# Optimization experiments

Measured on AMD Instinct MI355X. Metric: run time of the kernel, lower is better.

## Reference

```python
import jax, jax.numpy as jnp
import numpy as np

D_MODEL = 2048
HEADS = 16


def setup_inputs() -> dict:
    key = jax.random.key(0)
    ks = jax.random.split(key, 9)
    s = 1.0 / np.sqrt(D_MODEL)
    x = jax.random.normal(ks[0], (2, 2048, D_MODEL), dtype=jnp.float32)
    wq = jax.random.uniform(ks[1], (D_MODEL, D_MODEL), jnp.float32, -s, s)
    wk = jax.random.uniform(ks[2], (D_MODEL, D_MODEL), jnp.float32, -s, s)
    wv = jax.random.uniform(ks[3], (D_MODEL, D_MODEL), jnp.float32, -s, s)
    wo = jax.random.uniform(ks[4], (D_MODEL, D_MODEL), jnp.float32, -s, s)
    bq = jax.random.uniform(ks[5], (D_MODEL,), jnp.float32, -s, s)
    bk = jax.random.uniform(ks[6], (D_MODEL,), jnp.float32, -s, s)
    bv = jax.random.uniform(ks[7], (D_MODEL,), jnp.float32, -s, s)
    bo = jax.random.uniform(ks[8], (D_MODEL,), jnp.float32, -s, s)
    return {"x": x, "wq": wq, "bq": bq, "wk": wk, "bk": bk,
            "wv": wv, "bv": bv, "wo": wo, "bo": bo}


def _split(t, heads):
    b, s, d = t.shape
    return t.reshape(b, s, heads, d // heads).transpose(0, 2, 1, 3)  # [b,h,s,dh]


def reference(x, wq, bq, wk, bk, wv, bv, wo, bo):
    q = x @ wq.T + bq
    k = x @ wk.T + bk
    v = x @ wv.T + bv
    q, k, v = _split(q, HEADS), _split(k, HEADS), _split(v, HEADS)
    dh = q.shape[-1]
    scale = 1.0 / np.sqrt(dh).astype(np.float32)
    score = jnp.einsum('bhqd,bhkd->bhqk', q, k) * scale  # [b,h,s,s]
    score = jax.nn.softmax(score.astype(jnp.float32), axis=-1).astype(q.dtype)
    out = jnp.einsum('bhqk,bhkd->bhqd', score, v)
    b, h, s, _ = out.shape
    out = out.transpose(0, 2, 1, 3).reshape(b, s, h * dh)
    return out @ wo.T + bo
```

## Files before the change

kernel.cpp:

```cpp
#include <hip/hip_runtime.h>
#include <cstdint>
#include <cstddef>

#define D_MODEL 2048
#define SEQ 2048
#define BATCH 2
#define HEADS 16
#define DH 128
#define MROWS (BATCH * SEQ)

typedef __attribute__((ext_vector_type(8))) short short8;
typedef __attribute__((ext_vector_type(4))) float f32x4;
typedef __attribute__((ext_vector_type(16))) float f32x16;
typedef __attribute__((ext_vector_type(2))) unsigned int uint2e;

__device__ __forceinline__ unsigned short f2bf(float f) {
    unsigned int u = __builtin_bit_cast(unsigned int, f);
    u += 0x7fffu + ((u >> 16) & 1u);
    return (unsigned short)(u >> 16);
}

__device__ __forceinline__ unsigned int cvt_pk_bf16(float lo, float hi) {
    unsigned int w;
    asm("v_cvt_pk_bf16_f32 %0, %1, %2" : "=v"(w) : "v"(lo), "v"(hi));
    return w;
}

__device__ __forceinline__ void swap32(unsigned int& x, unsigned int& y) {
#if __has_builtin(__builtin_amdgcn_permlane32_swap)
    uint2e r = __builtin_amdgcn_permlane32_swap(x, y, false, false);
    x = r[0]; y = r[1];
#else
    const int hi = (threadIdx.x >> 5) & 1;
    const unsigned int gx = (unsigned int)__shfl_xor((int)x, 32);
    const unsigned int gy = (unsigned int)__shfl_xor((int)y, 32);
    const unsigned int nx = hi ? gy : x;
    const unsigned int ny = hi ? y : gx;
    x = nx; y = ny;
#endif
}

__device__ __forceinline__ void gload_lds16(const unsigned short* g, unsigned short* l) {
    __builtin_amdgcn_global_load_lds(
        (const __attribute__((address_space(1))) void*)g,
        (__attribute__((address_space(3))) void*)l, 16, 0, 0);
}

__global__ __launch_bounds__(256) void cvt_all(const float* __restrict__ x,
                                               const float* __restrict__ wq,
                                               const float* __restrict__ wk,
                                               const float* __restrict__ wv,
                                               const float* __restrict__ wo,
                                               unsigned short* __restrict__ out) {
    constexpr int PX = (MROWS * D_MODEL) / 4;
    constexpr int PW = (D_MODEL * D_MODEL) / 4;
    int i = blockIdx.x * 256 + threadIdx.x;
    const float* s;
    int off;
    if (i < PX) { s = x; off = i; }
    else {
        const int j = i - PX;
        const int sel = j / PW;
        off = j - sel * PW;
        s = sel == 0 ? wq : sel == 1 ? wk : sel == 2 ? wv : wo;
    }
    const float4 v = reinterpret_cast<const float4*>(s)[off];
    ushort4 o;
    o.x = f2bf(v.x); o.y = f2bf(v.y); o.z = f2bf(v.z); o.w = f2bf(v.w);
    reinterpret_cast<ushort4*>(out)[i] = o;
}

__global__ __launch_bounds__(512, 2)
void gemm8qk(const unsigned short* __restrict__ A,
             const unsigned short* __restrict__ W0,
             const unsigned short* __restrict__ W1,
             const float* __restrict__ b0f,
             const float* __restrict__ b1f,
             unsigned short* __restrict__ O0,
             unsigned short* __restrict__ O1) {
    constexpr int BK = 64;
    constexpr int K = D_MODEL;
    constexpr int NT_N = 16;
    constexpr int NWG = 16 * NT_N;
    __shared__ unsigned short As[2][16384];
    __shared__ unsigned short Bs[2][16384];

    const int tid  = threadIdx.x;
    const int lane = tid & 63;
    const int wid  = tid >> 6;

    const int wk = (blockIdx.x & 7) * (NWG >> 3) + (blockIdx.x >> 3);
    const int nt = wk % NT_N;
    const int mt = wk / NT_N;
    const int m0 = mt * 256;
    const int nsel = nt >> 3;
    const int nloc = (nt & 7) * 256;

    const unsigned short* Bw = nsel ? W1 : W0;
    const float* bias = nsel ? b1f : b0f;

    const int srow = tid >> 3;
    const int sch  = tid & 7;
    const int ssw  = (sch ^ (srow & 7)) * 8;
    const int sd   = srow * 64 + sch * 8;
    const unsigned short* aS[4];
    const unsigned short* bS[4];
#pragma unroll
    for (int j = 0; j < 4; ++j) {
        aS[j] = A  + (size_t)(m0 + j * 64 + srow) * K + ssw;
        bS[j] = Bw + (size_t)(nloc + j * 64 + srow) * K + ssw;
    }

    const int fr = lane & 15, fg = lane >> 4;
    const int wm = wid >> 2, wn = wid & 3;
    int aoffs[2], boffs[2];
#pragma unroll
    for (int ks = 0; ks < 2; ++ks) {
        const int sw = ((ks * 4 + fg) ^ (fr & 7)) * 8;
        aoffs[ks] = (wm * 128 + fr) * 64 + sw;
        boffs[ks] = (wn * 64 + fr) * 64 + sw;
    }

    f32x4 acc[8][4] = {};

#define STG_F(SET, T)                                                \
    gload_lds16(aS[0] + (T) * BK, &As[SET][0 * 4096 + sd]);          \
    gload_lds16(aS[1] + (T) * BK, &As[SET][1 * 4096 + sd]);          \
    gload_lds16(bS[0] + (T) * BK, &Bs[SET][0 * 4096 + sd]);          \
    gload_lds16(bS[1] + (T) * BK, &Bs[SET][1 * 4096 + sd]);
#define STG_L(SET, T)                                                \
    gload_lds16(aS[2] + (T) * BK, &As[SET][2 * 4096 + sd]);          \
    gload_lds16(aS[3] + (T) * BK, &As[SET][3 * 4096 + sd]);          \
    gload_lds16(bS[2] + (T) * BK, &Bs[SET][2 * 4096 + sd]);          \
    gload_lds16(bS[3] + (T) * BK, &Bs[SET][3 * 4096 + sd]);
#define RD_A(DST, SET, HB)                                           \
    _Pragma("unroll") for (int mi = 0; mi < 4; ++mi)                 \
    _Pragma("unroll") for (int ks = 0; ks < 2; ++ks)                 \
        DST[mi][ks] = *(const short8*)&As[SET][(HB) + mi * 1024 + aoffs[ks]];
#define RD_B(DST, SET, NB)                                           \
    _Pragma("unroll") for (int ni = 0; ni < 2; ++ni)                 \
    _Pragma("unroll") for (int ks = 0; ks < 2; ++ks)                 \
        DST[ni][ks] = *(const short8*)&Bs[SET][((NB) + ni) * 1024 + boffs[ks]];
#define PH_MFMA(AF, BF, MB, NB)                                      \
    __builtin_amdgcn_s_barrier();                                    \
    asm volatile("s_waitcnt lgkmcnt(0)" ::: "memory");               \
    __builtin_amdgcn_sched_barrier(0);                               \
    __builtin_amdgcn_s_setprio(1);                                   \
    _Pragma("unroll") for (int ks = 0; ks < 2; ++ks)                 \
    _Pragma("unroll") for (int mi = 0; mi < 4; ++mi)                 \
    _Pragma("unroll") for (int ni = 0; ni < 2; ++ni)                 \
        acc[(MB) + mi][(NB) + ni] = __builtin_amdgcn_mfma_f32_16x16x32_bf16( \
            AF[mi][ks], BF[ni][ks], acc[(MB) + mi][(NB) + ni], 0, 0, 0);     \
    __builtin_amdgcn_s_setprio(0);                                   \
    __builtin_amdgcn_s_barrier();

    STG_F(0, 0)
    STG_L(0, 0)
    STG_F(1, 1)
    asm volatile("s_waitcnt vmcnt(4)" ::: "memory");
    __builtin_amdgcn_s_barrier();

#pragma unroll 1
    for (int j = 0; j < 16; ++j) {
        const int t0 = 2 * j;
        const bool more = (j < 15);
        short8 aF[4][2], aG[4][2], b01[2][2], b23[2][2];
        RD_A(aF, 0, 0)
        RD_B(b01, 0, 0)
        STG_L(1, t0 + 1)
        PH_MFMA(aF, b01, 0, 0)
        RD_B(b23, 0, 2)
        PH_MFMA(aF, b23, 0, 2)
        RD_A(aG, 0, 4096)
        PH_MFMA(aG, b23, 4, 2)
        if (more) {
            STG_F(0, t0 + 2)
            asm volatile("s_waitcnt vmcnt(4)" ::: "memory");
        } else {
            asm volatile("s_waitcnt vmcnt(0)" ::: "memory");
        }
        PH_MFMA(aG, b01, 4, 0)
        RD_A(aF, 1, 0)
        RD_B(b01, 1, 0)
        if (more) { STG_L(0, t0 + 2) }
        PH_MFMA(aF, b01, 0, 0)
        RD_B(b23, 1, 2)
        PH_MFMA(aF, b23, 0, 2)
        RD_A(aG, 1, 4096)
        PH_MFMA(aG, b23, 4, 2)
        if (more) {
            STG_F(1, t0 + 3)
            asm volatile("s_waitcnt vmcnt(4)" ::: "memory");
        }
        PH_MFMA(aG, b01, 4, 0)
    }
#undef STG_F
#undef STG_L
#undef RD_A
#undef RD_B
#undef PH_MFMA

    unsigned short* Co = nsel ? O1 : O0;
#pragma unroll
    for (int mi = 0; mi < 8; ++mi)
#pragma unroll
        for (int ni = 0; ni < 4; ++ni) {
            const int col = nloc + wn * 64 + ni * 16 + fr;
            const float bv = bias[col];
#pragma unroll
            for (int r = 0; r < 4; ++r) {
                const int row = m0 + wm * 128 + mi * 16 + fg * 4 + r;
                Co[(size_t)row * D_MODEL + col] = f2bf(acc[mi][ni][r] + bv);
            }
        }
}

__global__ __launch_bounds__(512, 2)
void gemmV(const unsigned short* __restrict__ Wv,
           const unsigned short* __restrict__ X,
           const float* __restrict__ bvf,
           unsigned short* __restrict__ VT) {
    constexpr int BK = 64;
    constexpr int K = D_MODEL;
    constexpr int NTILES = K / BK;
    constexpr int NWG = 256;
    __shared__ unsigned short As[3][128 * BK];
    __shared__ unsigned short Bs[3][256 * BK];

    const int tid  = threadIdx.x;
    const int lane = tid & 63;
    const int wid  = tid >> 6;

    const int wk = (blockIdx.x & 7) * (NWG >> 3) + (blockIdx.x >> 3);
    const int nt = wk & 15;
    const int mt = wk >> 4;
    const int m0 = mt * 128;
    const int n0 = nt * 256;

    const int srow = tid >> 3;
    const int sch  = tid & 7;
    const int ssw  = (sch ^ (srow & 7)) * 8;
    const int sd   = srow * 64 + sch * 8;
    const unsigned short* aS[2];
#pragma unroll
    for (int j = 0; j < 2; ++j) aS[j] = Wv + (size_t)(m0 + j * 64 + srow) * K + ssw;
    const unsigned short* bS[4];
#pragma unroll
    for (int j = 0; j < 4; ++j) bS[j] = X + (size_t)(n0 + j * 64 + srow) * K + ssw;

    const int fr = lane & 15, fg = lane >> 4;
    const int wm = wid >> 2, wn = wid & 3;
    int aoff[4][2], boff[4][2];
#pragma unroll
    for (int i = 0; i < 4; ++i)
#pragma unroll
        for (int ks = 0; ks < 2; ++ks) {
            const int sw = ((ks * 4 + fg) ^ (fr & 7)) * 8;
            aoff[i][ks] = (wm * 64 + i * 16 + fr) * BK + sw;
            boff[i][ks] = (wn * 64 + i * 16 + fr) * BK + sw;
        }

    f32x4 acc[4][4] = {};

    unsigned short *pA0 = As[0], *pA1 = As[1], *pA2 = As[2];
    unsigned short *pB0 = Bs[0], *pB1 = Bs[1], *pB2 = Bs[2];

#define STG_AV(P, T) { _Pragma("unroll") for (int j = 0; j < 2; ++j) \
        gload_lds16(aS[j] + (T) * BK, (P) + j * 4096 + sd); }
#define STG_BV(P, T) { _Pragma("unroll") for (int j = 0; j < 4; ++j) \
        gload_lds16(bS[j] + (T) * BK, (P) + j * 4096 + sd); }

    STG_AV(pA0, 0) STG_BV(pB0, 0)
    STG_AV(pA1, 1) STG_BV(pB1, 1)
    asm volatile("s_waitcnt vmcnt(6)" ::: "memory");
    __builtin_amdgcn_s_barrier();

#pragma unroll 1
    for (int t = 0; t < NTILES; ++t) {
        const bool more = (t + 2 < NTILES);
        short8 aF[4][2], bF0[2][2];
#pragma unroll
        for (int mi = 0; mi < 4; ++mi)
#pragma unroll
            for (int ks = 0; ks < 2; ++ks)
                aF[mi][ks] = *(const short8*)&pA0[aoff[mi][ks]];
#pragma unroll
        for (int ni = 0; ni < 2; ++ni)
#pragma unroll
            for (int ks = 0; ks < 2; ++ks)
                bF0[ni][ks] = *(const short8*)&pB0[boff[ni][ks]];
        if (more) { STG_AV(pA2, t + 2) STG_BV(pB2, t + 2) }
        asm volatile("s_waitcnt lgkmcnt(0)" ::: "memory");
        __builtin_amdgcn_sched_barrier(0);
        __builtin_amdgcn_s_setprio(1);
#pragma unroll
        for (int ks = 0; ks < 2; ++ks)
#pragma unroll
            for (int mi = 0; mi < 4; ++mi)
#pragma unroll
                for (int ni = 0; ni < 2; ++ni)
                    acc[mi][ni] = __builtin_amdgcn_mfma_f32_16x16x32_bf16(
                        aF[mi][ks], bF0[ni][ks], acc[mi][ni], 0, 0, 0);
        __builtin_amdgcn_s_setprio(0);
        short8 bG[2][2];
#pragma unroll
        for (int ni = 0; ni < 2; ++ni)
#pragma unroll
            for (int ks = 0; ks < 2; ++ks)
                bG[ni][ks] = *(const short8*)&pB0[boff[2 + ni][ks]];
        asm volatile("s_waitcnt lgkmcnt(0)" ::: "memory");
        __builtin_amdgcn_sched_barrier(0);
        __builtin_amdgcn_s_setprio(1);
#pragma unroll
        for (int ks = 0; ks < 2; ++ks)
#pragma unroll
            for (int mi = 0; mi < 4; ++mi)
#pragma unroll
                for (int ni = 0; ni < 2; ++ni)
                    acc[mi][2 + ni] = __builtin_amdgcn_mfma_f32_16x16x32_bf16(
                        aF[mi][ks], bG[ni][ks], acc[mi][2 + ni], 0, 0, 0);
        __builtin_amdgcn_s_setprio(0);
        if (more) asm volatile("s_waitcnt vmcnt(6)" ::: "memory");
        else      asm volatile("s_waitcnt vmcnt(0)" ::: "memory");
        __builtin_amdgcn_s_barrier();
        unsigned short* tA = pA0; pA0 = pA1; pA1 = pA2; pA2 = tA;
        unsigned short* tB = pB0; pB0 = pB1; pB1 = pB2; pB2 = tB;
    }
#undef STG_AV
#undef STG_BV

#pragma unroll
    for (int mi = 0; mi < 4; ++mi)
#pragma unroll
        for (int r = 0; r < 4; ++r) {
            const int row = m0 + wm * 64 + mi * 16 + fg * 4 + r;
            const float bv = bvf[row];
#pragma unroll
            for (int ni = 0; ni < 4; ++ni) {
                const int col = n0 + wn * 64 + ni * 16 + fr;
                VT[(size_t)row * MROWS + col] = f2bf(acc[mi][ni][r] + bv);
            }
        }
}

__global__ __launch_bounds__(512, 2)
void gemmT1(const unsigned short* __restrict__ A,
            const unsigned short* __restrict__ W0,
            const float* __restrict__ b0f,
            float* __restrict__ OF) {
    constexpr int BM = 256, BN = 128, BK = 64;
    constexpr int K = D_MODEL;
    constexpr int NTILES = K / BK;
    constexpr int NT_N = 16;
    constexpr int NWG = (MROWS / BM) * NT_N;
    __shared__ unsigned short As[3][BM * BK];
    __shared__ unsigned short Bs[3][BN * BK];

    const int tid  = threadIdx.x;
    const int lane = tid & 63;
    const int wid  = tid >> 6;

    const int wk = (blockIdx.x & 7) * (NWG >> 3) + (blockIdx.x >> 3);
    const int nt = wk % NT_N;
    const int mt = wk / NT_N;
    const int m0 = mt * BM;
    const int n0 = nt * BN;

    const int srow = tid >> 3;
    const int sch  = tid & 7;
    const int ssw  = (sch ^ (srow & 7)) * 8;
    const int sd   = srow * 64 + sch * 8;
    const unsigned short* aS[4];
#pragma unroll
    for (int j = 0; j < 4; ++j) aS[j] = A + (size_t)(m0 + j * 64 + srow) * K + ssw;
    const unsigned short* bS[2];
#pragma unroll
    for (int j = 0; j < 2; ++j) bS[j] = W0 + (size_t)(n0 + j * 64 + srow) * K + ssw;

    const int fr = lane & 15, fg = lane >> 4;
    const int wm = wid >> 1, wn = wid & 1;
    int aoff[4][2], boff[4][2];
#pragma unroll
    for (int mi = 0; mi < 4; ++mi)
#pragma unroll
        for (int ks = 0; ks < 2; ++ks) {
            aoff[mi][ks] = (wm * 64 + mi * 16 + fr) * BK + ((ks * 4 + fg) ^ (fr & 7)) * 8;
            boff[mi][ks] = (wn * 64 + mi * 16 + fr) * BK + ((ks * 4 + fg) ^ (fr & 7)) * 8;
        }

    f32x4 acc[4][4] = {};

    unsigned short *pA0 = As[0], *pA1 = As[1], *pA2 = As[2];
    unsigned short *pB0 = Bs[0], *pB1 = Bs[1], *pB2 = Bs[2];

#define STG_A3(P, T) { _Pragma("unroll") for (int j = 0; j < 4; ++j) \
        gload_lds16(aS[j] + (T) * BK, (P) + j * 4096 + sd); }
#define STG_B3(P, T) { _Pragma("unroll") for (int j = 0; j < 2; ++j) \
        gload_lds16(bS[j] + (T) * BK, (P) + j * 4096 + sd); }

    STG_A3(pA0, 0) STG_B3(pB0, 0)
    STG_A3(pA1, 1) STG_B3(pB1, 1)
    asm volatile("s_waitcnt vmcnt(6)" ::: "memory");
    __builtin_amdgcn_s_barrier();

#pragma unroll 1
    for (int t = 0; t < NTILES; ++t) {
        const bool more = (t + 2 < NTILES);
        short8 aF[4][2], bF0[2][2];
#pragma unroll
        for (int mi = 0; mi < 4; ++mi)
#pragma unroll
            for (int ks = 0; ks < 2; ++ks)
                aF[mi][ks] = *(const short8*)&pA0[aoff[mi][ks]];
#pragma unroll
        for (int ni = 0; ni < 2; ++ni)
#pragma unroll
            for (int ks = 0; ks < 2; ++ks)
                bF0[ni][ks] = *(const short8*)&pB0[boff[ni][ks]];
        if (more) { STG_A3(pA2, t + 2) STG_B3(pB2, t + 2) }
        asm volatile("s_waitcnt lgkmcnt(0)" ::: "memory");
        __builtin_amdgcn_sched_barrier(0);
        __builtin_amdgcn_s_setprio(1);
#pragma unroll
        for (int ks = 0; ks < 2; ++ks)
#pragma unroll
            for (int mi = 0; mi < 4; ++mi)
#pragma unroll
                for (int ni = 0; ni < 2; ++ni)
                    acc[mi][ni] = __builtin_amdgcn_mfma_f32_16x16x32_bf16(
                        aF[mi][ks], bF0[ni][ks], acc[mi][ni], 0, 0, 0);
        __builtin_amdgcn_s_setprio(0);
        short8 bG[2][2];
#pragma unroll
        for (int ni = 0; ni < 2; ++ni)
#pragma unroll
            for (int ks = 0; ks < 2; ++ks)
                bG[ni][ks] = *(const short8*)&pB0[boff[2 + ni][ks]];
        asm volatile("s_waitcnt lgkmcnt(0)" ::: "memory");
        __builtin_amdgcn_sched_barrier(0);
        __builtin_amdgcn_s_setprio(1);
#pragma unroll
        for (int ks = 0; ks < 2; ++ks)
#pragma unroll
            for (int mi = 0; mi < 4; ++mi)
#pragma unroll
                for (int ni = 0; ni < 2; ++ni)
                    acc[mi][2 + ni] = __builtin_amdgcn_mfma_f32_16x16x32_bf16(
                        aF[mi][ks], bG[ni][ks], acc[mi][2 + ni], 0, 0, 0);
        __builtin_amdgcn_s_setprio(0);
        if (more) asm volatile("s_waitcnt vmcnt(6)" ::: "memory");
        else      asm volatile("s_waitcnt vmcnt(0)" ::: "memory");
        __builtin_amdgcn_s_barrier();
        unsigned short* tA = pA0; pA0 = pA1; pA1 = pA2; pA2 = tA;
        unsigned short* tB = pB0; pB0 = pB1; pB1 = pB2; pB2 = tB;
    }
#undef STG_A3
#undef STG_B3

#pragma unroll
    for (int mi = 0; mi < 4; ++mi)
#pragma unroll
        for (int ni = 0; ni < 4; ++ni) {
            const int col = n0 + wn * 64 + ni * 16 + fr;
            const float bv = b0f[col];
#pragma unroll
            for (int r = 0; r < 4; ++r) {
                const int row = m0 + wm * 64 + mi * 16 + fg * 4 + r;
                OF[(size_t)row * D_MODEL + col] = acc[mi][ni][r] + bv;
            }
        }
}

__global__ __launch_bounds__(256, 2)
void flash_attn3(const unsigned short* __restrict__ Q, const unsigned short* __restrict__ Kg,
                 const unsigned short* __restrict__ VT, unsigned short* __restrict__ O) {
    constexpr int KVB = 64;
    constexpr int NT = SEQ / KVB;
    __shared__ unsigned short Ks[2 * KVB * DH];
    __shared__ unsigned short Vs[2 * DH * KVB];

    const int tid  = threadIdx.x;
    const int lane = tid & 63;
    const int wid  = tid >> 6;
    const int l31  = lane & 31;
    const int hi   = lane >> 5;

    const int swz = (blockIdx.x & 7) * 64 + (blockIdx.x >> 3);
    const int qt = swz & 15;
    const int bh = swz >> 4;
    const int b = bh >> 4, h = bh & 15;
    const int qrow = qt * 128 + wid * 32 + l31;

    const unsigned short* Qp = Q + ((size_t)b * SEQ + qrow) * D_MODEL + h * DH;
    const unsigned short* Kp = Kg + (size_t)b * SEQ * D_MODEL + h * DH;
    const unsigned short* Vp = VT + (size_t)(h * DH) * MROWS + (size_t)b * SEQ;

    short8 qf[8];
#pragma unroll
    for (int kk = 0; kk < 8; ++kk)
        qf[kk] = *(const short8*)(Qp + kk * 16 + hi * 8);

    f32x16 acc[4] = {};
    float m_run = -1e30f, l_run = 0.f;
    const float Cc = 0.088388347648318447f * 1.4426950408889634f;
    const float THR = 8.0f / Cc;

    int co[8];
#pragma unroll
    for (int kk = 0; kk < 8; ++kk) co[kk] = ((kk * 2 + hi) ^ (l31 & 7)) * 8;

    int kroff[4], vroff[4];
#pragma unroll
    for (int q = 0; q < 4; ++q) {
        const int row_l = wid * 16 + q * 4 + (lane >> 4);
        kroff[q] = row_l * D_MODEL + ((lane & 15) ^ (row_l & 7)) * 8;
        const int d_l = wid * 32 + q * 8 + (lane >> 3);
        vroff[q] = d_l * MROWS + ((lane & 7) ^ (d_l & 7)) * 8;
    }
    unsigned short* KsW = Ks + (wid * 16) * DH;
    unsigned short* VsW = Vs + (wid * 32) * KVB;

#pragma unroll
    for (int q = 0; q < 4; ++q) {
        gload_lds16(Kp + kroff[q], KsW + q * 4 * DH);
        gload_lds16(Vp + vroff[q], VsW + q * 8 * KVB);
    }
    __syncthreads();

#pragma unroll 1
    for (int t = 0; t < NT; ++t) {
        const int cur = t & 1;
        if (t + 1 < NT) {
            const unsigned short* Kt = Kp + (size_t)((t + 1) * KVB) * D_MODEL;
            const unsigned short* Vt = Vp + (t + 1) * KVB;
            unsigned short* kd = KsW + (cur ^ 1) * (KVB * DH);
            unsigned short* vd = VsW + (cur ^ 1) * (DH * KVB);
#pragma unroll
            for (int q = 0; q < 4; ++q) {
                gload_lds16(Kt + kroff[q], kd + q * 4 * DH);
                gload_lds16(Vt + vroff[q], vd + q * 8 * KVB);
            }
        }
        const unsigned short* Kc = Ks + cur * (KVB * DH);
        const unsigned short* Vc = Vs + cur * (DH * KVB);

        f32x16 st0 = {}, st1 = {};
        __builtin_amdgcn_s_setprio(1);
#pragma unroll
        for (int kk = 0; kk < 8; ++kk) {
            const short8 kf0 = *(const short8*)&Kc[l31 * DH + co[kk]];
            const short8 kf1 = *(const short8*)&Kc[(32 + l31) * DH + co[kk]];
            st0 = __builtin_amdgcn_mfma_f32_32x32x16_bf16(kf0, qf[kk], st0, 0, 0, 0);
            st1 = __builtin_amdgcn_mfma_f32_32x32x16_bf16(kf1, qf[kk], st1, 0, 0, 0);
        }
        __builtin_amdgcn_s_setprio(0);

        float lm = -1e30f;
#pragma unroll
        for (int r = 0; r < 16; ++r) lm = fmaxf(lm, fmaxf(st0[r], st1[r]));
        {
            unsigned int a = __builtin_bit_cast(unsigned int, lm), bb = a;
            swap32(a, bb);
            lm = fmaxf(lm, __builtin_bit_cast(float, hi ? a : bb));
        }
        if (__any(lm > m_run + THR)) {
            const float mn = fmaxf(m_run, lm);
            const float sf = __builtin_amdgcn_exp2f((m_run - mn) * Cc);
            m_run = mn;
            l_run *= sf;
#pragma unroll
            for (int db = 0; db < 4; ++db)
#pragma unroll
                for (int r = 0; r < 16; ++r) acc[db][r] *= sf;
        }
        const float mc = m_run * Cc;
        float p0[16], p1[16];
        float ps = 0.f;
#pragma unroll
        for (int r = 0; r < 16; ++r) {
            p0[r] = __builtin_amdgcn_exp2f(__builtin_fmaf(st0[r], Cc, -mc));
            p1[r] = __builtin_amdgcn_exp2f(__builtin_fmaf(st1[r], Cc, -mc));
            ps += p0[r] + p1[r];
        }
        {
            unsigned int a = __builtin_bit_cast(unsigned int, ps), bb = a;
            swap32(a, bb);
            ps += __builtin_bit_cast(float, hi ? a : bb);
        }
        l_run += ps;

        unsigned int W0[8], W1[8];
#pragma unroll
        for (int tt = 0; tt < 8; ++tt) {
            W0[tt] = cvt_pk_bf16(p0[2 * tt], p0[2 * tt + 1]);
            W1[tt] = cvt_pk_bf16(p1[2 * tt], p1[2 * tt + 1]);
        }
        swap32(W0[0], W0[2]); swap32(W0[1], W0[3]);
        swap32(W0[4], W0[6]); swap32(W0[5], W0[7]);
        swap32(W1[0], W1[2]); swap32(W1[1], W1[3]);
        swap32(W1[4], W1[6]); swap32(W1[5], W1[7]);
        short8 pf[4];
        {
            uint4 f;
            f.x = W0[0]; f.y = W0[1]; f.z = W0[2]; f.w = W0[3];
            pf[0] = __builtin_bit_cast(short8, f);
            f.x = W0[4]; f.y = W0[5]; f.z = W0[6]; f.w = W0[7];
            pf[1] = __builtin_bit_cast(short8, f);
            f.x = W1[0]; f.y = W1[1]; f.z = W1[2]; f.w = W1[3];
            pf[2] = __builtin_bit_cast(short8, f);
            f.x = W1[4]; f.y = W1[5]; f.z = W1[6]; f.w = W1[7];
            pf[3] = __builtin_bit_cast(short8, f);
        }

        __builtin_amdgcn_s_setprio(1);
#pragma unroll
        for (int db = 0; db < 4; ++db) {
#pragma unroll
            for (int kk16 = 0; kk16 < 4; ++kk16) {
                const short8 vf = *(const short8*)&Vc[(db * 32 + l31) * KVB + co[kk16]];
                acc[db] = __builtin_amdgcn_mfma_f32_32x32x16_bf16(vf, pf[kk16], acc[db], 0, 0, 0);
            }
        }
        __builtin_amdgcn_s_setprio(0);
        __syncthreads();
    }

    const float inv_l = 1.0f / l_run;
    unsigned short* Op = O + ((size_t)b * SEQ + qrow) * D_MODEL + h * DH;
#pragma unroll
    for (int db = 0; db < 4; ++db)
#pragma unroll
        for (int g = 0; g < 4; ++g) {
            ushort4 o4;
            o4.x = f2bf(acc[db][4 * g + 0] * inv_l);
            o4.y = f2bf(acc[db][4 * g + 1] * inv_l);
            o4.z = f2bf(acc[db][4 * g + 2] * inv_l);
            o4.w = f2bf(acc[db][4 * g + 3] * inv_l);
            *(ushort4*)(Op + db * 32 + g * 8 + hi * 4) = o4;
        }
}

extern "C" void kernel_launch(void* const* d_in, const int* in_sizes, int n_in,
                              void* d_out, int out_size, void* d_ws, size_t ws_size,
                              hipStream_t stream) {
    (void)in_sizes; (void)n_in; (void)out_size; (void)ws_size;
    const float* x  = (const float*)d_in[0];
    const float* wq = (const float*)d_in[1];
    const float* bq = (const float*)d_in[2];
    const float* wk = (const float*)d_in[3];
    const float* bk = (const float*)d_in[4];
    const float* wv = (const float*)d_in[5];
    const float* bv = (const float*)d_in[6];
    const float* wo = (const float*)d_in[7];
    const float* bo = (const float*)d_in[8];
    float* out = (float*)d_out;

    unsigned short* ws = (unsigned short*)d_ws;
    const size_t NX = (size_t)MROWS * D_MODEL;
    const size_t NW = (size_t)D_MODEL * D_MODEL;
    unsigned short* xb  = ws;
    unsigned short* wqb = xb + NX;
    unsigned short* wkb = wqb + NW;
    unsigned short* wvb = wkb + NW;
    unsigned short* wob = wvb + NW;
    unsigned short* Qb  = wob + NW;
    unsigned short* Kb  = Qb + NX;
    unsigned short* VTb = Kb + NX;
    unsigned short* Ab  = VTb + NX;

    const unsigned cvt_blocks = (unsigned)((NX + 4 * NW) / 1024);
    cvt_all<<<cvt_blocks, 256, 0, stream>>>(x, wq, wk, wv, wo, xb);

    gemm8qk<<<256, 512, 0, stream>>>(xb, wqb, wkb, bq, bk, Qb, Kb);
    gemmV<<<256, 512, 0, stream>>>(wvb, xb, bv, VTb);

    flash_attn3<<<512, 256, 0, stream>>>(Qb, Kb, VTb, Ab);

    gemmT1<<<256, 512, 0, stream>>>(Ab, wob, bo, out);
}
```

Measured before the change: 247.0 us.

## Merge Q/K and V projection GEMMs into one 768-block launch

Replaces the separate 256x256-tile Q/K GEMM and the V-transpose GEMM with a single kernel that uses the 128x256 triple-buffered pipeline from gemmV for all three projections. Block index picks the job (Q, K or V^T), and the bias is applied per-column or per-row depending on the job. This removes one launch and the tail between the two kernels, and gives 768 blocks for better load balance. In exchange Q/K now run on the smaller tile with less data reuse per block than the tuned 256x256 kernel.

```diff
diff --git a/kernel.cpp b/kernel.cpp
--- a/kernel.cpp
+++ b/kernel.cpp
@@ -71,171 +71,50 @@
 }
 
 __global__ __launch_bounds__(512, 2)
-void gemm8qk(const unsigned short* __restrict__ A,
-             const unsigned short* __restrict__ W0,
-             const unsigned short* __restrict__ W1,
-             const float* __restrict__ b0f,
-             const float* __restrict__ b1f,
-             unsigned short* __restrict__ O0,
-             unsigned short* __restrict__ O1) {
+void gemm3(const unsigned short* __restrict__ X,
+           const unsigned short* __restrict__ Wq,
+           const unsigned short* __restrict__ Wk,
+           const unsigned short* __restrict__ Wv,
+           const float* __restrict__ bq,
+           const float* __restrict__ bk,
+           const float* __restrict__ bv,
+           unsigned short* __restrict__ Qb,
+           unsigned short* __restrict__ Kb,
+           unsigned short* __restrict__ VTb) {
     constexpr int BK = 64;
     constexpr int K = D_MODEL;
-    constexpr int NT_N = 16;
-    constexpr int NWG = 16 * NT_N;
-    __shared__ unsigned short As[2][16384];
-    __shared__ unsigned short Bs[2][16384];
+    constexpr int NTILES = K / BK;
+    constexpr int NWG = 768;
+    __shared__ unsigned short As[3][128 * BK];
+    __shared__ unsigned short Bs[3][256 * BK];
 
     const int tid  = threadIdx.x;
     const int lane = tid & 63;
     const int wid  = tid >> 6;
 
-    const int wk = (blockIdx.x & 7) * (NWG >> 3) + (blockIdx.x >> 3);
-    const int nt = wk % NT_N;
-    const int mt = wk / NT_N;
-    const int m0 = mt * 256;
-    const int nsel = nt >> 3;
-    const int nloc = (nt & 7) * 256;
-
-    const unsigned short* Bw = nsel ? W1 : W0;
-    const float* bias = nsel ? b1f : b0f;
-
-    const int srow = tid >> 3;
-    const int sch  = tid & 7;
-    const int ssw  = (sch ^ (srow & 7)) * 8;
-    const int sd   = srow * 64 + sch * 8;
-    const unsigned short* aS[4];
-    const unsigned short* bS[4];
-#pragma unroll
-    for (int j = 0; j < 4; ++j) {
-        aS[j] = A  + (size_t)(m0 + j * 64 + srow) * K + ssw;
-        bS[j] = Bw + (size_t)(nloc + j * 64 + srow) * K + ssw;
-    }
-
-    const int fr = lane & 15, fg = lane >> 4;
-    const int wm = wid >> 2, wn = wid & 3;
-    int aoffs[2], boffs[2];
-#pragma unroll
-    for (int ks = 0; ks < 2; ++ks) {
-        const int sw = ((ks * 4 + fg) ^ (fr & 7)) * 8;
-        aoffs[ks] = (wm * 128 + fr) * 64 + sw;
-        boffs[ks] = (wn * 64 + fr) * 64 + sw;
-    }
-
-    f32x4 acc[8][4] = {};
-
-#define STG_F(SET, T)                                                \
-    gload_lds16(aS[0] + (T) * BK, &As[SET][0 * 4096 + sd]);          \
-    gload_lds16(aS[1] + (T) * BK, &As[SET][1 * 4096 + sd]);          \
-    gload_lds16(bS[0] + (T) * BK, &Bs[SET][0 * 4096 + sd]);          \
-    gload_lds16(bS[1] + (T) * BK, &Bs[SET][1 * 4096 + sd]);
-#define STG_L(SET, T)                                                \
-    gload_lds16(aS[2] + (T) * BK, &As[SET][2 * 4096 + sd]);          \
-    gload_lds16(aS[3] + (T) * BK, &As[SET][3 * 4096 + sd]);          \
-    gload_lds16(bS[2] + (T) * BK, &Bs[SET][2 * 4096 + sd]);          \
-    gload_lds16(bS[3] + (T) * BK, &Bs[SET][3 * 4096 + sd]);
-#define RD_A(DST, SET, HB)                                           \
-    _Pragma("unroll") for (int mi = 0; mi < 4; ++mi)                 \
-    _Pragma("unroll") for (int ks = 0; ks < 2; ++ks)                 \
-        DST[mi][ks] = *(const short8*)&As[SET][(HB) + mi * 1024 + aoffs[ks]];
-#define RD_B(DST, SET, NB)                                           \
-    _Pragma("unroll") for (int ni = 0; ni < 2; ++ni)                 \
-    _Pragma("unroll") for (int ks = 0; ks < 2; ++ks)                 \
-        DST[ni][ks] = *(const short8*)&Bs[SET][((NB) + ni) * 1024 + boffs[ks]];
-#define PH_MFMA(AF, BF, MB, NB)                                      \
-    __builtin_amdgcn_s_barrier();                                    \
-    asm volatile("s_waitcnt lgkmcnt(0)" ::: "memory");               \
-    __builtin_amdgcn_sched_barrier(0);                               \
-    __builtin_amdgcn_s_setprio(1);                                   \
-    _Pragma("unroll") for (int ks = 0; ks < 2; ++ks)                 \
-    _Pragma("unroll") for (int mi = 0; mi < 4; ++mi)                 \
-    _Pragma("unroll") for (int ni = 0; ni < 2; ++ni)                 \
-        acc[(MB) + mi][(NB) + ni] = __builtin_amdgcn_mfma_f32_16x16x32_bf16( \
-            AF[mi][ks], BF[ni][ks], acc[(MB) + mi][(NB) + ni], 0, 0, 0);     \
-    __builtin_amdgcn_s_setprio(0);                                   \
-    __builtin_amdgcn_s_barrier();
-
-    STG_F(0, 0)
-    STG_L(0, 0)
-    STG_F(1, 1)
-    asm volatile("s_waitcnt vmcnt(4)" ::: "memory");
-    __builtin_amdgcn_s_barrier();
-
-#pragma unroll 1
-    for (int j = 0; j < 16; ++j) {
-        const int t0 = 2 * j;
-        const bool more = (j < 15);
-        short8 aF[4][2], aG[4][2], b01[2][2], b23[2][2];
-        RD_A(aF, 0, 0)
-        RD_B(b01, 0, 0)
-        STG_L(1, t0 + 1)
-        PH_MFMA(aF, b01, 0, 0)
-        RD_B(b23, 0, 2)
-        PH_MFMA(aF, b23, 0, 2)
-        RD_A(aG, 0, 4096)
-        PH_MFMA(aG, b23, 4, 2)
-        if (more) {
-            STG_F(0, t0 + 2)
-            asm volatile("s_waitcnt vmcnt(4)" ::: "memory");
-        } else {
-            asm volatile("s_waitcnt vmcnt(0)" ::: "memory");
-        }
-        PH_MFMA(aG, b01, 4, 0)
-        RD_A(aF, 1, 0)
-        RD_B(b01, 1, 0)
-        if (more) { STG_L(0, t0 + 2) }
-        PH_MFMA(aF, b01, 0, 0)
-        RD_B(b23, 1, 2)
-        PH_MFMA(aF, b23, 0, 2)
-        RD_A(aG, 1, 4096)
-        PH_MFMA(aG, b23, 4, 2)
-        if (more) {
-            STG_F(1, t0 + 3)
-            asm volatile("s_waitcnt vmcnt(4)" ::: "memory");
-        }
-        PH_MFMA(aG, b01, 4, 0)
-    }
-#undef STG_F
-#undef STG_L
-#undef RD_A
-#undef RD_B
-#undef PH_MFMA
-
-    unsigned short* Co = nsel ? O1 : O0;
-#pragma unroll
-    for (int mi = 0; mi < 8; ++mi)
-#pragma unroll
-        for (int ni = 0; ni < 4; ++ni) {
-            const int col = nloc + wn * 64 + ni * 16 + fr;
-            const float bv = bias[col];
-#pragma unroll
-            for (int r = 0; r < 4; ++r) {
-                const int row = m0 + wm * 128 + mi * 16 + fg * 4 + r;
-                Co[(size_t)row * D_MODEL + col] = f2bf(acc[mi][ni][r] + bv);
-            }
-        }
-}
-
-__global__ __launch_bounds__(512, 2)
-void gemmV(const unsigned short* __restrict__ Wv,
-           const unsigned short* __restrict__ X,
-           const float* __restrict__ bvf,
-           unsigned short* __restrict__ VT) {
-    constexpr int BK = 64;
-    constexpr int K = D_MODEL;
-    constexpr int NTILES = K / BK;
-    constexpr int NWG = 256;
-    __shared__ unsigned short As[3][128 * BK];
-    __shared__ unsigned short Bs[3][256 * BK];
-
-    const int tid  = threadIdx.x;
-    const int lane = tid & 63;
-    const int wid  = tid >> 6;
-
-    const int wk = (blockIdx.x & 7) * (NWG >> 3) + (blockIdx.x >> 3);
-    const int nt = wk & 15;
-    const int mt = wk >> 4;
-    const int m0 = mt * 128;
-    const int n0 = nt * 256;
+    const int swz = (blockIdx.x & 7) * (NWG >> 3) + (blockIdx.x >> 3);
+    const int job   = swz >> 8;
+    const int local = swz & 255;
+
+    const unsigned short* aBase;
+    const unsigned short* bBase;
+    const float* bias;
+    unsigned short* cBase;
+    int ldc, m0, n0;
+    bool brow;
+    if (job == 2) {
+        m0 = (local >> 4) * 128;
+        n0 = (local & 15) * 256;
+        aBase = Wv; bBase = X; bias = bv; cBase = VTb; ldc = MROWS; brow = true;
+    } else {
+        m0 = (local >> 3) * 128;
+        n0 = (local & 7) * 256;
+        aBase = X;
+        bBase = job ? Wk : Wq;
+        bias  = job ? bk : bq;
+        cBase = job ? Kb : Qb;
+        ldc = D_MODEL; brow = false;
+    }
 
     const int srow = tid >> 3;
     const int sch  = tid & 7;
@@ -243,10 +122,10 @@
     const int sd   = srow * 64 + sch * 8;
     const unsigned short* aS[2];
 #pragma unroll
-    for (int j = 0; j < 2; ++j) aS[j] = Wv + (size_t)(m0 + j * 64 + srow) * K + ssw;
+    for (int j = 0; j < 2; ++j) aS[j] = aBase + (size_t)(m0 + j * 64 + srow) * K + ssw;
     const unsigned short* bS[4];
 #pragma unroll
-    for (int j = 0; j < 4; ++j) bS[j] = X + (size_t)(n0 + j * 64 + srow) * K + ssw;
+    for (int j = 0; j < 4; ++j) bS[j] = bBase + (size_t)(n0 + j * 64 + srow) * K + ssw;
 
     const int fr = lane & 15, fg = lane >> 4;
     const int wm = wid >> 2, wn = wid & 3;
@@ -334,11 +213,12 @@
 #pragma unroll
         for (int r = 0; r < 4; ++r) {
             const int row = m0 + wm * 64 + mi * 16 + fg * 4 + r;
-            const float bv = bvf[row];
+            const float brv = brow ? bias[row] : 0.f;
 #pragma unroll
             for (int ni = 0; ni < 4; ++ni) {
                 const int col = n0 + wn * 64 + ni * 16 + fr;
-                VT[(size_t)row * MROWS + col] = f2bf(acc[mi][ni][r] + bv);
+                const float bvv = brow ? brv : bias[col];
+                cBase[(size_t)row * ldc + col] = f2bf(acc[mi][ni][r] + bvv);
             }
         }
 }
@@ -671,8 +551,7 @@
     const unsigned cvt_blocks = (unsigned)((NX + 4 * NW) / 1024);
     cvt_all<<<cvt_blocks, 256, 0, stream>>>(x, wq, wk, wv, wo, xb);
 
-    gemm8qk<<<256, 512, 0, stream>>>(xb, wqb, wkb, bq, bk, Qb, Kb);
-    gemmV<<<256, 512, 0, stream>>>(wvb, xb, bv, VTb);
+    gemm3<<<768, 512, 0, stream>>>(xb, wqb, wkb, wvb, bq, bk, bv, Qb, Kb, VTb);
 
     flash_attn3<<<512, 256, 0, stream>>>(Qb, Kb, VTb, Ab);
 
```

Result: slower. 271.9 us (+10.1%).
